# Performance work log

Hardware: AMD Instinct MI355X
Metric: run time of the kernel (lower is better)

## Reference

```python
import jax
import jax.numpy as jnp
from jax import lax
import numpy as np

L, B, D_IN, D = 1024, 16, 2048, 2048
K = 3  # n_in == n_out -> k = 3, highway uses x directly


def setup_inputs() -> dict:
    key = jax.random.key(0)
    k1, k2 = jax.random.split(key)
    x = jax.random.normal(k1, (L, B, D_IN), dtype=jnp.float32)
    c0 = jnp.zeros((B, D), dtype=jnp.float32)
    # learned params: projection weight (n_in, n_out*k) and bias (2*n_out)
    weight = jax.random.normal(k2, (D_IN, D * K), dtype=jnp.float32) * (1.0 / np.sqrt(D_IN))
    bias = jnp.zeros((2 * D,), dtype=jnp.float32)
    return {"x": x, "c0": c0, "weight": weight, "bias": bias}


def reference(x, c0, weight, bias):
    # x: [L, B, n_in], c0: [B, d], weight: [n_in, d*3], bias: [2*d]
    Llen, Bsz, _ = x.shape
    d = c0.shape[-1]
    u = jnp.einsum("lbi,ik->lbk", x, weight).reshape(Llen, Bsz, d, K)
    u0 = u[..., 0]                                   # candidate
    g1 = jax.nn.sigmoid(u[..., 1] + bias[:d])        # forget gate
    g2 = jax.nn.sigmoid(u[..., 2] + bias[d:])        # highway/reset gate

    # sequential recurrence: c_t = (c_{t-1} - u0_t) * g1_t + u0_t
    def step(c_prev, inp):
        u0_t, g1_t = inp
        c_t = (c_prev - u0_t) * g1_t + u0_t
        return c_t, c_t

    c_last, cs = lax.scan(step, c0, (u0, g1))
    # h_t = (tanh(c_t) - x_t) * g2_t + x_t   (use_tanh=1, k=3 highway on x)
    h = (jnp.tanh(cs) - x) * g2 + x
    return h, c_last
```

## Files before the change

kernel.cpp:

```cpp
#include <hip/hip_runtime.h>
#include <hip/hip_bf16.h>
#include <cstdint>

#define L_SEQ 1024
#define BSZ   16
#define DIN   2048
#define DD    2048
#define MROWS (L_SEQ * BSZ)
#define NCOLS (3 * DD)
#define BKT   64
#define NT    (DIN / BKT)

typedef __attribute__((ext_vector_type(8))) short  short8;
typedef __attribute__((ext_vector_type(4))) float  f32x4;
typedef __attribute__((ext_vector_type(4))) ushort ushort4v;

typedef const __attribute__((address_space(1))) void* gas_ptr;
typedef __attribute__((address_space(3))) void*       las_ptr;

#define GLOAD16(g, l) __builtin_amdgcn_global_load_lds((gas_ptr)(g), (las_ptr)(l), 16, 0, 0)

__device__ __forceinline__ float bf2f(ushort u) {
    return __uint_as_float(((uint32_t)u) << 16);
}
__device__ __forceinline__ ushort f2bf(float f) {
    uint32_t u = __float_as_uint(f);
    uint32_t r = u + 0x7FFFu + ((u >> 16) & 1u);
    return (ushort)(r >> 16);
}

__global__ __launch_bounds__(256) void pre_kernel(const f32x4* __restrict__ x4,
                                                  ushort4v* __restrict__ xb4,
                                                  const float* __restrict__ W,
                                                  ushort* __restrict__ WT) {
    __shared__ float tile[64][65];
    int bid = blockIdx.x;
    if (bid < 2048) {
        int i = bid * 256 + threadIdx.x;
        const int n4 = MROWS * DIN / 4;
        const int stride = 2048 * 256;
        for (; i < n4; i += stride) {
            f32x4 v = x4[i];
            ushort4v o;
            o.x = f2bf(v.x); o.y = f2bf(v.y); o.z = f2bf(v.z); o.w = f2bf(v.w);
            xb4[i] = o;
        }
    } else {
        int b2 = bid - 2048;
        int k0 = (b2 & 31) * 64;
        int n0 = (b2 >> 5) * 64;
        int c  = threadIdx.x & 63;
        int r0 = threadIdx.x >> 6;
#pragma unroll
        for (int rr = 0; rr < 16; ++rr) {
            int r = r0 + rr * 4;
            tile[r][c] = W[(size_t)(k0 + r) * NCOLS + n0 + c];
        }
        __syncthreads();
#pragma unroll
        for (int rr = 0; rr < 16; ++rr) {
            int r = r0 + rr * 4;
            int n = n0 + r;
            int nprime = (n % 3) * DD + (n / 3);
            WT[(size_t)nprime * DIN + k0 + c] = f2bf(tile[c][r]);
        }
    }
}

#define SLOT(b, s) (&lds8[(((b) << 2) + (s)) * 8192])

#define STAGE_A(b, h, kt) do {                                                   \
    const ushort* _g = Ab + (size_t)((h) * 64 + idx) * DIN + (kt) * BKT + akc;   \
    ushort* _l = SLOT(b, (h)) + tid * 8;                                         \
    GLOAD16(_g, _l);                                                             \
    GLOAD16(_g + (size_t)128 * DIN, _l + 4096);                                  \
} while (0)

#define STAGE_B(b, h2, kt) do {                                                  \
    const ushort* _g0 = Bb + (size_t)(brow0 + (h2) * 32) * DIN + (kt) * BKT + akc;\
    const ushort* _g1 = Bb + (size_t)(brow1 + (h2) * 32) * DIN + (kt) * BKT + akc;\
    ushort* _l = SLOT(b, 2 + (h2)) + tid * 8;                                    \
    GLOAD16(_g0, _l);                                                            \
    GLOAD16(_g1, _l + 4096);                                                     \
} while (0)

#define STAGE_A_P(b, h, p) do {                                                  \
    ushort* _l = SLOT(b, (h)) + tid * 8;                                         \
    GLOAD16((p), _l);                                                            \
    GLOAD16((p) + (size_t)128 * DIN, _l + 4096);                                 \
} while (0)

#define STAGE_B_P(b, h2, p0, p1) do {                                            \
    ushort* _l = SLOT(b, 2 + (h2)) + tid * 8;                                    \
    GLOAD16((p0), _l);                                                           \
    GLOAD16((p1), _l + 4096);                                                    \
} while (0)

#define LD_A(b, h) do { const ushort* _s = SLOT(b, (h)) + a_rb;                  \
    _Pragma("unroll") for (int _m = 0; _m < 4; ++_m) {                           \
        aF[_m][0] = *(const short8*)(_s + _m * 1024 + cs0);                      \
        aF[_m][1] = *(const short8*)(_s + _m * 1024 + cs1); }                    \
} while (0)

#define LD_B(b, h2, bF) do { const ushort* _s = SLOT(b, 2 + (h2)) + b_rb;        \
    _Pragma("unroll") for (int _n = 0; _n < 2; ++_n) {                           \
        bF[_n][0] = *(const short8*)(_s + _n * 1024 + cs0);                      \
        bF[_n][1] = *(const short8*)(_s + _n * 1024 + cs1); }                    \
} while (0)

#define MM(mb, bF, nb) do {                                                      \
    __builtin_amdgcn_s_setprio(1);                                               \
    _Pragma("unroll") for (int _m = 0; _m < 4; ++_m)                             \
    _Pragma("unroll") for (int _n = 0; _n < 2; ++_n) {                           \
        acc[(mb)+_m][(nb)+_n] = __builtin_amdgcn_mfma_f32_16x16x32_bf16(         \
            bF[_n][0], aF[_m][0], acc[(mb)+_m][(nb)+_n], 0, 0, 0);               \
        acc[(mb)+_m][(nb)+_n] = __builtin_amdgcn_mfma_f32_16x16x32_bf16(         \
            bF[_n][1], aF[_m][1], acc[(mb)+_m][(nb)+_n], 0, 0, 0); }             \
    __builtin_amdgcn_s_setprio(0);                                               \
    __builtin_amdgcn_sched_barrier(0);                                           \
} while (0)

#define BARF() do { __builtin_amdgcn_sched_barrier(0);                           \
    __builtin_amdgcn_s_barrier();                                                \
    __builtin_amdgcn_sched_barrier(0); } while (0)

__global__ __launch_bounds__(512, 2) void sru_gemm8(const ushort* __restrict__ A,
                                                    const ushort* __restrict__ Bt,
                                                    const float*  __restrict__ bias,
                                                    ushort* __restrict__ u0,
                                                    ushort* __restrict__ g1,
                                                    ushort* __restrict__ g2) {
    __shared__ alignas(16) ushort lds8[65536];

    int bid = blockIdx.x;
    int swz = (bid & 7) * 192 + (bid >> 3);
    int bm0 = (swz / 24) * 256;
    int bn0 = (swz % 24) * 256;

    int tid  = threadIdx.x;
    int wave = tid >> 6, lane = tid & 63;
    int wm = wave >> 2, wn = wave & 3;

    int idx    = tid >> 3;
    int schunk = (tid & 7) ^ (idx & 7);
    int akc    = schunk * 8;
    int brow0  = (idx >> 5) * 64 + (idx & 31);
    int brow1  = ((idx >> 5) + 2) * 64 + (idx & 31);
    const ushort* Ab = A  + (size_t)bm0 * DIN;
    const ushort* Bb = Bt + (size_t)bn0 * DIN;

    const ushort* pA1  = Ab + (size_t)(64 + idx) * DIN + akc + BKT;
    const ushort* pA0  = Ab + (size_t)idx        * DIN + akc + 2 * BKT;
    const ushort* pB1a = Bb + (size_t)(brow0 + 32) * DIN + akc + BKT;
    const ushort* pB1b = Bb + (size_t)(brow1 + 32) * DIN + akc + BKT;
    const ushort* pB0a = Bb + (size_t)brow0 * DIN + akc + 2 * BKT;
    const ushort* pB0b = Bb + (size_t)brow1 * DIN + akc + 2 * BKT;

    int lrow = lane & 15, lk = lane >> 4, lx = lane & 7;
    int cs0  = ((0 + lk) ^ lx) * 8;
    int cs1  = ((4 + lk) ^ lx) * 8;
    int a_rb = (wm * 64 + lrow) * 64;
    int b_rb = (wn * 32 + lrow) * 64;

    f32x4 acc[8][4];
    f32x4 zero = {0.f, 0.f, 0.f, 0.f};
#pragma unroll
    for (int i = 0; i < 8; ++i)
#pragma unroll
        for (int j = 0; j < 4; ++j) acc[i][j] = zero;

    STAGE_A(0, 0, 0); STAGE_A(0, 1, 0); STAGE_B(0, 0, 0); STAGE_B(0, 1, 0);
    STAGE_A(1, 0, 1); STAGE_B(1, 0, 1);
    asm volatile("s_waitcnt vmcnt(4)" ::: "memory");
    BARF();

    short8 aF[4][2], bF0[2][2], bF1[2][2];

    for (int t = 0; t < NT; ++t) {
        int cur = t & 1, nxt = cur ^ 1;
        LD_A(cur, 0); LD_B(cur, 0, bF0);
        STAGE_A_P(nxt, 1, pA1);
        BARF(); MM(0, bF0, 0); BARF();
        LD_B(cur, 1, bF1);
        STAGE_B_P(nxt, 1, pB1a, pB1b);
        BARF(); MM(0, bF1, 2); BARF();
        LD_A(cur, 1);
        STAGE_A_P(cur, 0, pA0);
        BARF(); MM(4, bF0, 0); BARF();
        STAGE_B_P(cur, 0, pB0a, pB0b);
        asm volatile("s_waitcnt vmcnt(4)" ::: "memory");
        BARF(); MM(4, bF1, 2); BARF();
        pA1 += BKT; pA0 += BKT; pB1a += BKT; pB1b += BKT; pB0a += BKT; pB0b += BKT;
    }
    asm volatile("s_waitcnt vmcnt(0)" ::: "memory");

    int region = bn0 >> 11;
    int colb = (bn0 & (DD - 1)) + wn * 64 + ((lane >> 4) << 2);
    int rowm = bm0 + wm * 128 + (lane & 15);
    if (region == 0) {
#pragma unroll
        for (int j = 0; j < 4; ++j)
#pragma unroll
            for (int i = 0; i < 4; ++i) {
                f32x4 v = acc[i][j];
                uint32_t lo, hi;
                asm("v_cvt_pk_bf16_f32 %0, %1, %2" : "=v"(lo) : "v"(v[0]), "v"(v[1]));
                asm("v_cvt_pk_bf16_f32 %0, %1, %2" : "=v"(hi) : "v"(v[2]), "v"(v[3]));
                uint2 pk; pk.x = lo; pk.y = hi;
                *(uint2*)&u0[(size_t)(rowm + i * 16) * DD + colb + j * 16] = pk;
                f32x4 w = acc[4 + i][j];
                asm("v_cvt_pk_bf16_f32 %0, %1, %2" : "=v"(lo) : "v"(w[0]), "v"(w[1]));
                asm("v_cvt_pk_bf16_f32 %0, %1, %2" : "=v"(hi) : "v"(w[2]), "v"(w[3]));
                pk.x = lo; pk.y = hi;
                *(uint2*)&u0[(size_t)(rowm + 64 + i * 16) * DD + colb + j * 16] = pk;
            }
    } else {
        const float* bp = bias + (size_t)(region - 1) * DD;
        ushort* gp = (region == 1) ? g1 : g2;
#pragma unroll
        for (int j = 0; j < 4; ++j) {
            float4 bv = *(const float4*)&bp[colb + j * 16];
#pragma unroll
            for (int i = 0; i < 8; ++i) {
                f32x4 v = acc[i][j];
                float s0 = 1.f / (1.f + __expf(-(v[0] + bv.x)));
                float s1 = 1.f / (1.f + __expf(-(v[1] + bv.y)));
                float s2 = 1.f / (1.f + __expf(-(v[2] + bv.z)));
                float s3 = 1.f / (1.f + __expf(-(v[3] + bv.w)));
                uint32_t lo, hi;
                asm("v_cvt_pk_bf16_f32 %0, %1, %2" : "=v"(lo) : "v"(s0), "v"(s1));
                asm("v_cvt_pk_bf16_f32 %0, %1, %2" : "=v"(hi) : "v"(s2), "v"(s3));
                uint2 pk; pk.x = lo; pk.y = hi;
                int rr = rowm + (i >> 2) * 64 + (i & 3) * 16;
                *(uint2*)&gp[(size_t)rr * DD + colb + j * 16] = pk;
            }
        }
    }
}

__global__ __launch_bounds__(64) void sru_rec(const ushort* __restrict__ u0,
                                              const ushort* __restrict__ g1,
                                              const ushort* __restrict__ g2,
                                              const ushort* __restrict__ xb,
                                              const float*  __restrict__ c0,
                                              float* __restrict__ h,
                                              float* __restrict__ c_last) {
    int t = blockIdx.x * 64 + threadIdx.x;
    float c = c0[t];
#pragma unroll 16
    for (int l = 0; l < L_SEQ; ++l) {
        int ix = l * (BSZ * DD) + t;
        float uu  = bf2f(u0[ix]);
        float gg1 = bf2f(g1[ix]);
        float gg2 = bf2f(g2[ix]);
        float xx  = bf2f(xb[ix]);
        c = (c - uu) * gg1 + uu;
        float e  = __expf(-2.f * fabsf(c));
        float th = (1.f - e) / (1.f + e);
        th = copysignf(th, c);
        h[ix] = (th - xx) * gg2 + xx;
    }
    c_last[t] = c;
}

extern "C" void kernel_launch(void* const* d_in, const int* in_sizes, int n_in,
                              void* d_out, int out_size, void* d_ws, size_t ws_size,
                              hipStream_t stream) {
    const float* x    = (const float*)d_in[0];
    const float* c0   = (const float*)d_in[1];
    const float* W    = (const float*)d_in[2];
    const float* bias = (const float*)d_in[3];
    float* out = (float*)d_out;

    char* ws = (char*)d_ws;
    ushort* xb = (ushort*)(ws);
    ushort* WT = (ushort*)(ws + 67108864);
    ushort* u0 = (ushort*)(ws + 92274688);
    ushort* g1 = (ushort*)(ws + 159383552);
    ushort* g2 = (ushort*)(ws + 226492416);

    hipLaunchKernelGGL(pre_kernel, dim3(5120), dim3(256), 0, stream,
                       (const f32x4*)x, (ushort4v*)xb, W, WT);
    hipLaunchKernelGGL(sru_gemm8, dim3(1536), dim3(512), 0, stream, xb, WT, bias, u0, g1, g2);
    hipLaunchKernelGGL(sru_rec, dim3(512), dim3(64), 0, stream,
                       u0, g1, g2, xb, c0, out, out + (size_t)MROWS * DD);
}
```

Before: 576.8 us.

## Double-buffer A fragments and prefetch next tile's A during last MFMA block

Measured after the change: 572.3 us. No clear change (-0.8%).

```diff
diff --git a/kernel.cpp b/kernel.cpp
--- a/kernel.cpp
+++ b/kernel.cpp
@@ -84,22 +84,10 @@
     GLOAD16(_g1, _l + 4096);                                                     \
 } while (0)
 
-#define STAGE_A_P(b, h, p) do {                                                  \
-    ushort* _l = SLOT(b, (h)) + tid * 8;                                         \
-    GLOAD16((p), _l);                                                            \
-    GLOAD16((p) + (size_t)128 * DIN, _l + 4096);                                 \
-} while (0)
-
-#define STAGE_B_P(b, h2, p0, p1) do {                                            \
-    ushort* _l = SLOT(b, 2 + (h2)) + tid * 8;                                    \
-    GLOAD16((p0), _l);                                                           \
-    GLOAD16((p1), _l + 4096);                                                    \
-} while (0)
-
-#define LD_A(b, h) do { const ushort* _s = SLOT(b, (h)) + a_rb;                  \
+#define LD_A2(dst, b, h) do { const ushort* _s = SLOT(b, (h)) + a_rb;            \
     _Pragma("unroll") for (int _m = 0; _m < 4; ++_m) {                           \
-        aF[_m][0] = *(const short8*)(_s + _m * 1024 + cs0);                      \
-        aF[_m][1] = *(const short8*)(_s + _m * 1024 + cs1); }                    \
+        dst[_m][0] = *(const short8*)(_s + _m * 1024 + cs0);                     \
+        dst[_m][1] = *(const short8*)(_s + _m * 1024 + cs1); }                   \
 } while (0)
 
 #define LD_B(b, h2, bF) do { const ushort* _s = SLOT(b, 2 + (h2)) + b_rb;        \
@@ -108,14 +96,14 @@
         bF[_n][1] = *(const short8*)(_s + _n * 1024 + cs1); }                    \
 } while (0)
 
-#define MM(mb, bF, nb) do {                                                      \
+#define MM(mb, aR, bF, nb) do {                                                  \
     __builtin_amdgcn_s_setprio(1);                                               \
     _Pragma("unroll") for (int _m = 0; _m < 4; ++_m)                             \
     _Pragma("unroll") for (int _n = 0; _n < 2; ++_n) {                           \
         acc[(mb)+_m][(nb)+_n] = __builtin_amdgcn_mfma_f32_16x16x32_bf16(         \
-            bF[_n][0], aF[_m][0], acc[(mb)+_m][(nb)+_n], 0, 0, 0);               \
+            bF[_n][0], aR[_m][0], acc[(mb)+_m][(nb)+_n], 0, 0, 0);               \
         acc[(mb)+_m][(nb)+_n] = __builtin_amdgcn_mfma_f32_16x16x32_bf16(         \
-            bF[_n][1], aF[_m][1], acc[(mb)+_m][(nb)+_n], 0, 0, 0); }             \
+            bF[_n][1], aR[_m][1], acc[(mb)+_m][(nb)+_n], 0, 0, 0); }             \
     __builtin_amdgcn_s_setprio(0);                                               \
     __builtin_amdgcn_sched_barrier(0);                                           \
 } while (0)
@@ -149,13 +137,6 @@
     const ushort* Ab = A  + (size_t)bm0 * DIN;
     const ushort* Bb = Bt + (size_t)bn0 * DIN;
 
-    const ushort* pA1  = Ab + (size_t)(64 + idx) * DIN + akc + BKT;
-    const ushort* pA0  = Ab + (size_t)idx        * DIN + akc + 2 * BKT;
-    const ushort* pB1a = Bb + (size_t)(brow0 + 32) * DIN + akc + BKT;
-    const ushort* pB1b = Bb + (size_t)(brow1 + 32) * DIN + akc + BKT;
-    const ushort* pB0a = Bb + (size_t)brow0 * DIN + akc + 2 * BKT;
-    const ushort* pB0b = Bb + (size_t)brow1 * DIN + akc + 2 * BKT;
-
     int lrow = lane & 15, lk = lane >> 4, lx = lane & 7;
     int cs0  = ((0 + lk) ^ lx) * 8;
     int cs1  = ((4 + lk) ^ lx) * 8;
@@ -174,23 +155,27 @@
     asm volatile("s_waitcnt vmcnt(4)" ::: "memory");
     BARF();
 
-    short8 aF[4][2], bF0[2][2], bF1[2][2];
+    short8 aFA[4][2], aFB[4][2], bF0[2][2], bF1[2][2];
+    LD_A2(aFA, 0, 0);
+    __builtin_amdgcn_sched_barrier(0);
 
     for (int t = 0; t < NT; ++t) {
         int cur = t & 1, nxt = cur ^ 1;
-        LD_A(cur, 0); LD_B(cur, 0, bF0);
-        STAGE_A_P(nxt, 1, pA1);
-        BARF(); MM(0, bF0, 0); BARF();
+        LD_B(cur, 0, bF0);
         LD_B(cur, 1, bF1);
-        STAGE_B_P(nxt, 1, pB1a, pB1b);
-        BARF(); MM(0, bF1, 2); BARF();
-        LD_A(cur, 1);
-        STAGE_A_P(cur, 0, pA0);
-        BARF(); MM(4, bF0, 0); BARF();
-        STAGE_B_P(cur, 0, pB0a, pB0b);
+        STAGE_A(nxt, 1, t + 1);
+        BARF(); MM(0, aFA, bF0, 0); BARF();
+        LD_A2(aFB, cur, 1);
+        STAGE_B(nxt, 1, t + 1);
+        BARF(); MM(0, aFA, bF1, 2); BARF();
+        STAGE_A(cur, 0, t + 2);
+        BARF(); MM(4, aFB, bF0, 0); BARF();
+        STAGE_B(cur, 0, t + 2);
         asm volatile("s_waitcnt vmcnt(4)" ::: "memory");
-        BARF(); MM(4, bF1, 2); BARF();
-        pA1 += BKT; pA0 += BKT; pB1a += BKT; pB1b += BKT; pB0a += BKT; pB0b += BKT;
+        BARF();
+        LD_A2(aFA, nxt, 0);
+        MM(4, aFB, bF1, 2);
+        BARF();
     }
     asm volatile("s_waitcnt vmcnt(0)" ::: "memory");
 
```
